# Kernel tuning notes

Hardware: AMD Instinct MI355X
Metric: run time of the kernel (lower is better)

## Reference

```python
import jax, jax.numpy as jnp
import numpy as np

N_LAYERS = 32
D_CONV = 4
D_STATE = 16


def _ln(x, w, b, eps=1e-5):
    mu = jnp.mean(x, axis=-1, keepdims=True)
    var = jnp.mean((x - mu) ** 2, axis=-1, keepdims=True)
    return (x - mu) / jnp.sqrt(var + eps) * w + b


def _mamba(x, in_w, conv_w, conv_b, xproj_w, dt_w, dt_b, A_log, D_skip, out_w):
    # x: (B, L, d_model); standard Mamba mixer (mamba_ssm defaults)
    B, L, _ = x.shape
    d_inner = in_w.shape[0] // 2
    xz = jnp.einsum('bld,ed->ble', x, in_w)  # (B, L, 2*d_inner)
    xs, z = xz[..., :d_inner], xz[..., d_inner:]
    # causal depthwise conv1d (kernel D_CONV) + SiLU
    xp = jnp.pad(xs, ((0, 0), (D_CONV - 1, 0), (0, 0)))
    xc = conv_b + sum(conv_w[:, k] * xp[:, k:k + L, :] for k in range(D_CONV))
    xc = jax.nn.silu(xc)
    dt_rank = dt_w.shape[1]
    dbc = jnp.einsum('bld,nd->bln', xc, xproj_w)  # (B, L, dt_rank + 2*d_state)
    dt = jax.nn.softplus(jnp.einsum('blr,dr->bld', dbc[..., :dt_rank], dt_w) + dt_b)
    Bm = dbc[..., dt_rank:dt_rank + D_STATE]
    Cm = dbc[..., dt_rank + D_STATE:]
    A = -jnp.exp(A_log)  # (d_inner, d_state)

    def step(h, inp):
        dt_t, B_t, C_t, x_t = inp  # (B,d),(B,n),(B,n),(B,d)
        h = jnp.exp(dt_t[..., None] * A) * h + dt_t[..., None] * B_t[:, None, :] * x_t[..., None]
        return h, jnp.einsum('bdn,bn->bd', h, C_t)

    h0 = jnp.zeros((B, d_inner, D_STATE), x.dtype)
    _, ys = jax.lax.scan(step, h0, (jnp.swapaxes(dt, 0, 1), jnp.swapaxes(Bm, 0, 1),
                                    jnp.swapaxes(Cm, 0, 1), jnp.swapaxes(xc, 0, 1)))
    y = jnp.swapaxes(ys, 0, 1) + D_skip * xc
    y = y * jax.nn.silu(z)
    return jnp.einsum('bld,od->blo', y, out_w)


def _forward(hidden_states, proj_w, proj_b, query, ln_w, ln_b, in_w, conv_w, conv_b,
             xproj_w, dt_w, dt_b, A_log, D_skip, out_w, norm_w, norm_b, num_query_token):
    h = jnp.einsum('bli,di->bld', hidden_states, proj_w) + proj_b
    B = h.shape[0]
    h = jnp.concatenate([h, jnp.broadcast_to(query, (B, query.shape[1], query.shape[2]))], axis=1)

    def layer(carry, p):
        hs, res = carry
        lw, lb, iw, cw, cb, xw, dw, db, al, dsk, ow = p
        res = hs + res  # first layer: res starts at 0 == residual=None case
        hs = _mamba(_ln(res, lw, lb), iw, cw, cb, xw, dw, db, al, dsk, ow)
        return (hs, res), None

    (hs, res), _ = jax.lax.scan(layer, (h, jnp.zeros_like(h)),
                                (ln_w, ln_b, in_w, conv_w, conv_b, xproj_w, dt_w, dt_b, A_log, D_skip, out_w))
    out = _ln(hs + res, norm_w, norm_b)
    return out[:, -num_query_token:]


def setup_inputs():
    key = jax.random.key(0)
    B, L, input_dim, d_model, nq = 2, 256, 1408, 512, 7
    d_inner, dt_rank = 2 * d_model, 32  # ceil(d_model/16)
    ks = jax.random.split(key, 9)
    s = 0.02
    return {
        'hidden_states': jax.random.normal(ks[0], (B, L, input_dim), jnp.float32),
        'proj_w': jax.random.normal(ks[1], (d_model, input_dim), jnp.float32) * s,
        'proj_b': jnp.zeros((d_model,), jnp.float32),
        'query': jax.random.uniform(ks[2], (1, nq, d_model), jnp.float32),
        'ln_w': jnp.ones((N_LAYERS, d_model), jnp.float32),
        'ln_b': jnp.zeros((N_LAYERS, d_model), jnp.float32),
        'in_w': jax.random.normal(ks[3], (N_LAYERS, 2 * d_inner, d_model), jnp.float32) * s,
        'conv_w': jax.random.normal(ks[4], (N_LAYERS, d_inner, D_CONV), jnp.float32) * 0.1,
        'conv_b': jnp.zeros((N_LAYERS, d_inner), jnp.float32),
        'xproj_w': jax.random.normal(ks[5], (N_LAYERS, dt_rank + 2 * D_STATE, d_inner), jnp.float32) * s,
        'dt_w': jax.random.normal(ks[6], (N_LAYERS, d_inner, dt_rank), jnp.float32) * s,
        'dt_b': jax.random.normal(ks[7], (N_LAYERS, d_inner), jnp.float32) * 0.1 - 4.0,
        'A_log': jnp.log(jnp.broadcast_to(jnp.arange(1, D_STATE + 1, dtype=jnp.float32), (N_LAYERS, d_inner, D_STATE))),
        'D_skip': jnp.ones((N_LAYERS, d_inner), jnp.float32),
        'out_w': jax.random.normal(ks[8], (N_LAYERS, d_model, d_inner), jnp.float32) * s,
        'norm_w': jnp.ones((d_model,), jnp.float32),
        'norm_b': jnp.zeros((d_model,), jnp.float32),
        'num_query_token': nq,
    }


def reference(hidden_states, proj_w, proj_b, query, ln_w, ln_b, in_w, conv_w, conv_b,
              xproj_w, dt_w, dt_b, A_log, D_skip, out_w, norm_w, norm_b, num_query_token):
    return _forward(hidden_states, proj_w, proj_b, query, ln_w, ln_b, in_w, conv_w, conv_b,
                    xproj_w, dt_w, dt_b, A_log, D_skip, out_w, norm_w, norm_b, num_query_token)
```

## Files before the change

### kernel.cpp

```cpp
#include <hip/hip_runtime.h>

#define DM 512
#define DI 1024
#define LSEQ 263
#define NTOK 526
#define NLAYER 32
#define DTR 32
#define DSTATE 16

typedef __attribute__((ext_vector_type(8))) short bf16x8;
typedef __attribute__((ext_vector_type(4))) short bf16x4;
typedef __attribute__((ext_vector_type(4))) float f32x4;

__device__ __forceinline__ short f2bf(float f) {
  unsigned u = __float_as_uint(f);
  unsigned r = u + 0x7FFFu + ((u >> 16) & 1u);
  return (short)(r >> 16);
}
__device__ __forceinline__ float silu_f(float v) { return v / (1.f + __expf(-v)); }
__device__ __forceinline__ float softplus_f(float x) {
  return fmaxf(x, 0.f) + log1pf(__expf(-fabsf(x)));
}

template<int BM, int BN, int AM, int AN, int MODE>
__global__ __launch_bounds__(256) void gemm_k(
    const float* __restrict__ A, const float* __restrict__ Bw,
    float* __restrict__ C, const float* __restrict__ x0,
    const float* __restrict__ x1, int M, int N, int K)
{
  constexpr int WC = BN / (AN * 16);
  constexpr int TPRA = 256 / BM, EPA = 32 / TPRA;
  constexpr int TPRB = 256 / BN, EPB = 32 / TPRB;
  __shared__ short As[BM][40];
  __shared__ short Bs[BN][40];
  __shared__ float mu_s[BM], rs_s[BM];
  const int tid = threadIdx.x;
  const int lane = tid & 63;
  const int w = tid >> 6;
  const int wm = (w / WC) * (AM * 16), wn = (w % WC) * (AN * 16);
  const int m0 = blockIdx.y * BM, n0 = blockIdx.x * BN;
  const int arow = tid / TPRA, acol = (tid % TPRA) * EPA;
  const int brow = tid / TPRB, bcol = (tid % TPRB) * EPB;
  const int agr = m0 + arow;
  const size_t abase = (size_t)agr * K + acol;
  const size_t bbase = (size_t)(n0 + brow) * K + bcol;

  if constexpr (MODE == 1) {
    for (int r = w; r < BM; r += 4) {
      int row = m0 + r;
      float s = 0.f, ss = 0.f;
      if (row < M) {
        const float4* p = reinterpret_cast<const float4*>(A + (size_t)row * 512 + lane * 8);
        float4 v0 = p[0], v1 = p[1];
        s = v0.x + v0.y + v0.z + v0.w + v1.x + v1.y + v1.z + v1.w;
        ss = v0.x*v0.x + v0.y*v0.y + v0.z*v0.z + v0.w*v0.w
           + v1.x*v1.x + v1.y*v1.y + v1.z*v1.z + v1.w*v1.w;
      }
#pragma unroll
      for (int o = 1; o < 64; o <<= 1) { s += __shfl_xor(s, o); ss += __shfl_xor(ss, o); }
      if (lane == 0) {
        float mean = s * (1.f / 512.f);
        float var = ss * (1.f / 512.f) - mean * mean;
        mu_s[r] = mean;
        rs_s[r] = rsqrtf(var + 1e-5f);
      }
    }
    __syncthreads();
  }

  f32x4 acc[AM][AN] = {};
  float4 pa[2], pb[2], pw[2], pl[2];

  auto loadA = [&](int k0) {
    if (agr < M) {
      const float4* p = reinterpret_cast<const float4*>(A + abase + k0);
      pa[0] = p[0];
      if constexpr (EPA == 8) pa[1] = p[1];
    } else {
      pa[0] = make_float4(0.f, 0.f, 0.f, 0.f);
      pa[1] = make_float4(0.f, 0.f, 0.f, 0.f);
    }
    if constexpr (MODE == 1) {
      const float4* pwp = reinterpret_cast<const float4*>(x0 + k0 + acol);
      const float4* plp = reinterpret_cast<const float4*>(x1 + k0 + acol);
      pw[0] = pwp[0]; pw[1] = pwp[1];
      pl[0] = plp[0]; pl[1] = plp[1];
    }
  };
  auto loadB = [&](int k0) {
    const float4* p = reinterpret_cast<const float4*>(Bw + bbase + k0);
    pb[0] = p[0];
    if constexpr (EPB == 8) pb[1] = p[1];
  };
  auto stage = [&]() {
    float va[8];
    va[0]=pa[0].x; va[1]=pa[0].y; va[2]=pa[0].z; va[3]=pa[0].w;
    if constexpr (EPA == 8) { va[4]=pa[1].x; va[5]=pa[1].y; va[6]=pa[1].z; va[7]=pa[1].w; }
    if constexpr (MODE == 1) {
      float mu = mu_s[arow], rs = rs_s[arow];
      float wv[8] = {pw[0].x,pw[0].y,pw[0].z,pw[0].w,pw[1].x,pw[1].y,pw[1].z,pw[1].w};
      float bv[8] = {pl[0].x,pl[0].y,pl[0].z,pl[0].w,pl[1].x,pl[1].y,pl[1].z,pl[1].w};
#pragma unroll
      for (int j = 0; j < EPA; ++j) va[j] = (va[j] - mu) * rs * wv[j] + bv[j];
    }
    if constexpr (EPA == 8) {
      bf16x8 o;
#pragma unroll
      for (int j = 0; j < 8; ++j) o[j] = f2bf(va[j]);
      *reinterpret_cast<bf16x8*>(&As[arow][acol]) = o;
    } else {
      bf16x4 o;
#pragma unroll
      for (int j = 0; j < 4; ++j) o[j] = f2bf(va[j]);
      *reinterpret_cast<bf16x4*>(&As[arow][acol]) = o;
    }
    float vb[8];
    vb[0]=pb[0].x; vb[1]=pb[0].y; vb[2]=pb[0].z; vb[3]=pb[0].w;
    if constexpr (EPB == 8) { vb[4]=pb[1].x; vb[5]=pb[1].y; vb[6]=pb[1].z; vb[7]=pb[1].w; }
    if constexpr (EPB == 8) {
      bf16x8 o;
#pragma unroll
      for (int j = 0; j < 8; ++j) o[j] = f2bf(vb[j]);
      *reinterpret_cast<bf16x8*>(&Bs[brow][bcol]) = o;
    } else {
      bf16x4 o;
#pragma unroll
      for (int j = 0; j < 4; ++j) o[j] = f2bf(vb[j]);
      *reinterpret_cast<bf16x4*>(&Bs[brow][bcol]) = o;
    }
  };

  loadA(0); loadB(0);
  const int nk = K / 32;
  for (int kk = 0; kk < nk; ++kk) {
    stage();
    __syncthreads();
    if (kk + 1 < nk) { loadA((kk + 1) * 32); loadB((kk + 1) * 32); }
    bf16x8 af[AM], bfr[AN];
#pragma unroll
    for (int i = 0; i < AM; ++i)
      af[i] = *reinterpret_cast<const bf16x8*>(&As[wm + i * 16 + (lane & 15)][(lane >> 4) * 8]);
#pragma unroll
    for (int j = 0; j < AN; ++j)
      bfr[j] = *reinterpret_cast<const bf16x8*>(&Bs[wn + j * 16 + (lane & 15)][(lane >> 4) * 8]);
#pragma unroll
    for (int i = 0; i < AM; ++i)
#pragma unroll
      for (int j = 0; j < AN; ++j)
        acc[i][j] = __builtin_amdgcn_mfma_f32_16x16x32_bf16(af[i], bfr[j], acc[i][j], 0, 0, 0);
    __syncthreads();
  }

#pragma unroll
  for (int i = 0; i < AM; ++i)
#pragma unroll
    for (int j = 0; j < AN; ++j)
#pragma unroll
      for (int r = 0; r < 4; ++r) {
        int row = m0 + wm + i * 16 + ((lane >> 4) << 2) + r;
        int col = n0 + wn + j * 16 + (lane & 15);
        if (row < M) {
          float v = acc[i][j][r];
          if constexpr (MODE == 0) {
            v += x0[col];
            int orow = ((row >> 8) * LSEQ) + (row & 255);
            C[(size_t)orow * N + col] = v;
          } else if constexpr (MODE == 1) {
            C[(size_t)row * N + col] = v;
          } else {
            C[(size_t)row * N + col] += v;
          }
        }
      }
}

__global__ void set_query_kernel(const float* __restrict__ q, float* __restrict__ res) {
  int i = blockIdx.x * 256 + threadIdx.x;
  if (i >= 2 * 7 * DM) return;
  int b = i / (7 * DM);
  int rrem = i - b * 7 * DM;
  int t = rrem / DM, d = rrem - t * DM;
  res[((size_t)b * LSEQ + 256 + t) * DM + d] = q[t * DM + d];
}

__global__ __launch_bounds__(256) void prep_kernel(
    const float* __restrict__ xz,
    const float* __restrict__ conv_w, const float* __restrict__ conv_b,
    const float* __restrict__ xproj_w,
    const float* __restrict__ dt_w, const float* __restrict__ dt_b,
    const float* __restrict__ Dsk,
    float* __restrict__ dt, float* __restrict__ dtx,
    float* __restrict__ w1o, float* __restrict__ w0o,
    float* __restrict__ Bm, float* __restrict__ Cm)
{
  __shared__ float xcs[DI];
  __shared__ float dbc_s[64];
  __shared__ float sp_s[DI];
  const int blk = blockIdx.x;
  const int t = blk % LSEQ;
  const int tid = threadIdx.x;
  const int lane = tid & 63;
  const int w = tid >> 6;
  const int c0 = tid * 4;

  {
    const float4* cwp = reinterpret_cast<const float4*>(conv_w + (size_t)c0 * 4);
    float4 cw0 = cwp[0], cw1 = cwp[1], cw2 = cwp[2], cw3 = cwp[3];
    float4 cb4 = *reinterpret_cast<const float4*>(conv_b + c0);
    float4 D4  = *reinterpret_cast<const float4*>(Dsk + c0);
    float4 xr[4];
#pragma unroll
    for (int k = 0; k < 4; ++k) {
      if (t - 3 + k >= 0)
        xr[k] = *reinterpret_cast<const float4*>(xz + (size_t)(blk - 3 + k) * 2048 + c0);
      else
        xr[k] = make_float4(0.f, 0.f, 0.f, 0.f);
    }
    float xc0 = silu_f(cb4.x + cw0.x*xr[0].x + cw0.y*xr[1].x + cw0.z*xr[2].x + cw0.w*xr[3].x);
    float xc1 = silu_f(cb4.y + cw1.x*xr[0].y + cw1.y*xr[1].y + cw1.z*xr[2].y + cw1.w*xr[3].y);
    float xc2 = silu_f(cb4.z + cw2.x*xr[0].z + cw2.y*xr[1].z + cw2.z*xr[2].z + cw2.w*xr[3].z);
    float xc3 = silu_f(cb4.w + cw3.x*xr[0].w + cw3.y*xr[1].w + cw3.z*xr[2].w + cw3.w*xr[3].w);
    xcs[c0] = xc0; xcs[c0+1] = xc1; xcs[c0+2] = xc2; xcs[c0+3] = xc3;
    float4 zv = *reinterpret_cast<const float4*>(xz + (size_t)blk * 2048 + DI + c0);
    float g0 = silu_f(zv.x), g1 = silu_f(zv.y), g2 = silu_f(zv.z), g3 = silu_f(zv.w);
    *reinterpret_cast<float4*>(w1o + (size_t)blk * DI + c0) = make_float4(g0, g1, g2, g3);
    *reinterpret_cast<float4*>(w0o + (size_t)blk * DI + c0) =
        make_float4(D4.x*xc0*g0, D4.y*xc1*g1, D4.z*xc2*g2, D4.w*xc3*g3);
  }
  __syncthreads();
  {
#pragma unroll 2
    for (int nn = 0; nn < 16; ++nn) {
      int nidx = w * 16 + nn;
      const float4* wr = reinterpret_cast<const float4*>(xproj_w + (size_t)nidx * DI);
      float s = 0.f;
#pragma unroll
      for (int j = 0; j < 4; ++j) {
        float4 wv = wr[j * 64 + lane];
        float4 xv = *reinterpret_cast<const float4*>(&xcs[j * 256 + lane * 4]);
        s += wv.x*xv.x + wv.y*xv.y + wv.z*xv.z + wv.w*xv.w;
      }
#pragma unroll
      for (int o = 1; o < 64; o <<= 1) s += __shfl_xor(s, o);
      if (lane == 0) dbc_s[nidx] = s;
    }
  }
  __syncthreads();
  if (tid < 32) {
    float v = dbc_s[32 + tid];
    if (tid < 16) Bm[(size_t)blk * DSTATE + tid] = v;
    else          Cm[(size_t)blk * DSTATE + (tid - 16)] = v;
  }
  {
    const int rp = tid & 7;
    float4 dv = *reinterpret_cast<const float4*>(&dbc_s[rp * 4]);
#pragma unroll 4
    for (int it = 0; it < 32; ++it) {
      int c = it * 32 + (tid >> 3);
      float4 wv = *reinterpret_cast<const float4*>(dt_w + (size_t)c * DTR + rp * 4);
      float s = wv.x*dv.x + wv.y*dv.y + wv.z*dv.z + wv.w*dv.w;
      s += __shfl_xor(s, 1); s += __shfl_xor(s, 2); s += __shfl_xor(s, 4);
      if (rp == 0) sp_s[c] = s;
    }
  }
  __syncthreads();
  {
    float4 db4 = *reinterpret_cast<const float4*>(dt_b + c0);
    float sp0 = softplus_f(sp_s[c0+0] + db4.x);
    float sp1 = softplus_f(sp_s[c0+1] + db4.y);
    float sp2 = softplus_f(sp_s[c0+2] + db4.z);
    float sp3 = softplus_f(sp_s[c0+3] + db4.w);
    *reinterpret_cast<float4*>(dt  + (size_t)blk * DI + c0) = make_float4(sp0, sp1, sp2, sp3);
    *reinterpret_cast<float4*>(dtx + (size_t)blk * DI + c0) =
        make_float4(sp0*xcs[c0], sp1*xcs[c0+1], sp2*xcs[c0+2], sp3*xcs[c0+3]);
  }
}

__global__ __launch_bounds__(128) void scan_kernel(
    const float* __restrict__ dt, const float* __restrict__ dtx,
    const float* __restrict__ Bm, const float* __restrict__ Cm,
    const float* __restrict__ w1, const float* __restrict__ w0,
    const float* __restrict__ A_log, float* __restrict__ y)
{
  const int blk = blockIdx.x;
  const int b = blk >> 7, cg = blk & 127;
  const int tid = threadIdx.x;
  const int n = tid & 15, cl = tid >> 4;
  const int c = cg * 8 + cl;
  const float Av = -__expf(A_log[(size_t)c * DSTATE + n]);
  float h = 0.f;
  __shared__ float sdt[64][8], sdx[64][8], sw1[64][8], sw0[64][8], sy[64][8];
  __shared__ float sB[64][16], sC[64][16];
  const size_t rb = (size_t)b * LSEQ;
  for (int t0 = 0; t0 < LSEQ; t0 += 64) {
    const int tc = (LSEQ - t0 < 64) ? (LSEQ - t0) : 64;
    __syncthreads();
    for (int i = tid; i < tc * 8; i += 128) {
      int tl = i >> 3, cc = i & 7;
      size_t g = (rb + t0 + tl) * DI + cg * 8 + cc;
      sdt[tl][cc] = dt[g]; sdx[tl][cc] = dtx[g];
      sw1[tl][cc] = w1[g]; sw0[tl][cc] = w0[g];
    }
    for (int i = tid; i < tc * 16; i += 128) {
      int tl = i >> 4, cc = i & 15;
      size_t gb = (rb + t0 + tl) * DSTATE + cc;
      sB[tl][cc] = Bm[gb]; sC[tl][cc] = Cm[gb];
    }
    __syncthreads();
    int tl = 0;
    for (; tl + 4 <= tc; tl += 4) {
      float e0 = __expf(sdt[tl+0][cl] * Av);
      float e1 = __expf(sdt[tl+1][cl] * Av);
      float e2 = __expf(sdt[tl+2][cl] * Av);
      float e3 = __expf(sdt[tl+3][cl] * Av);
      float x0_ = sdx[tl+0][cl] * sB[tl+0][n];
      float x1_ = sdx[tl+1][cl] * sB[tl+1][n];
      float x2_ = sdx[tl+2][cl] * sB[tl+2][n];
      float x3_ = sdx[tl+3][cl] * sB[tl+3][n];
      h = fmaf(e0, h, x0_); float p0 = h * sC[tl+0][n];
      h = fmaf(e1, h, x1_); float p1 = h * sC[tl+1][n];
      h = fmaf(e2, h, x2_); float p2 = h * sC[tl+2][n];
      h = fmaf(e3, h, x3_); float p3 = h * sC[tl+3][n];
      p0 += __shfl_xor(p0, 1); p1 += __shfl_xor(p1, 1); p2 += __shfl_xor(p2, 1); p3 += __shfl_xor(p3, 1);
      p0 += __shfl_xor(p0, 2); p1 += __shfl_xor(p1, 2); p2 += __shfl_xor(p2, 2); p3 += __shfl_xor(p3, 2);
      p0 += __shfl_xor(p0, 4); p1 += __shfl_xor(p1, 4); p2 += __shfl_xor(p2, 4); p3 += __shfl_xor(p3, 4);
      p0 += __shfl_xor(p0, 8); p1 += __shfl_xor(p1, 8); p2 += __shfl_xor(p2, 8); p3 += __shfl_xor(p3, 8);
      if (n == 0) {
        sy[tl+0][cl] = fmaf(p0, sw1[tl+0][cl], sw0[tl+0][cl]);
        sy[tl+1][cl] = fmaf(p1, sw1[tl+1][cl], sw0[tl+1][cl]);
        sy[tl+2][cl] = fmaf(p2, sw1[tl+2][cl], sw0[tl+2][cl]);
        sy[tl+3][cl] = fmaf(p3, sw1[tl+3][cl], sw0[tl+3][cl]);
      }
    }
    for (; tl < tc; ++tl) {
      float e = __expf(sdt[tl][cl] * Av);
      float bx = sdx[tl][cl] * sB[tl][n];
      h = fmaf(e, h, bx);
      float p = h * sC[tl][n];
      p += __shfl_xor(p, 1); p += __shfl_xor(p, 2);
      p += __shfl_xor(p, 4); p += __shfl_xor(p, 8);
      if (n == 0) sy[tl][cl] = fmaf(p, sw1[tl][cl], sw0[tl][cl]);
    }
    __syncthreads();
    for (int i = tid; i < tc * 8; i += 128) {
      int tl2 = i >> 3, cc = i & 7;
      y[(rb + t0 + tl2) * DI + cg * 8 + cc] = sy[tl2][cc];
    }
  }
}

__global__ __launch_bounds__(256) void final_ln_kernel(
    const float* __restrict__ res, const float* __restrict__ w,
    const float* __restrict__ b_, float* __restrict__ out)
{
  const int blk = blockIdx.x;
  const int bb = blk / 7, q = blk % 7;
  const int tid = threadIdx.x;
  const size_t base = ((size_t)bb * LSEQ + 256 + q) * DM;
  float r0 = res[base + tid];
  float r1 = res[base + tid + 256];
  float s = r0 + r1, ss = r0 * r0 + r1 * r1;
#pragma unroll
  for (int o = 1; o < 64; o <<= 1) { s += __shfl_xor(s, o); ss += __shfl_xor(ss, o); }
  __shared__ float sb[4], ssb[4];
  if ((tid & 63) == 0) { sb[tid >> 6] = s; ssb[tid >> 6] = ss; }
  __syncthreads();
  s = sb[0] + sb[1] + sb[2] + sb[3];
  ss = ssb[0] + ssb[1] + ssb[2] + ssb[3];
  float mean = s * (1.f / DM);
  float var = ss * (1.f / DM) - mean * mean;
  float rstd = rsqrtf(var + 1e-5f);
  out[((size_t)bb * 7 + q) * DM + tid] = (r0 - mean) * rstd * w[tid] + b_[tid];
  out[((size_t)bb * 7 + q) * DM + tid + 256] = (r1 - mean) * rstd * w[tid + 256] + b_[tid + 256];
}

extern "C" void kernel_launch(void* const* d_in, const int* in_sizes, int n_in,
                              void* d_out, int out_size, void* d_ws, size_t ws_size,
                              hipStream_t stream)
{
  (void)in_sizes; (void)n_in; (void)out_size; (void)ws_size;
  const float* hidden  = (const float*)d_in[0];
  const float* proj_w  = (const float*)d_in[1];
  const float* proj_b  = (const float*)d_in[2];
  const float* query   = (const float*)d_in[3];
  const float* ln_w    = (const float*)d_in[4];
  const float* ln_b    = (const float*)d_in[5];
  const float* in_w    = (const float*)d_in[6];
  const float* conv_w  = (const float*)d_in[7];
  const float* conv_b  = (const float*)d_in[8];
  const float* xproj_w = (const float*)d_in[9];
  const float* dt_w    = (const float*)d_in[10];
  const float* dt_b    = (const float*)d_in[11];
  const float* A_log   = (const float*)d_in[12];
  const float* D_skip  = (const float*)d_in[13];
  const float* out_w   = (const float*)d_in[14];
  const float* norm_w  = (const float*)d_in[15];
  const float* norm_b  = (const float*)d_in[16];
  float* out = (float*)d_out;

  float* p = (float*)d_ws;
  float* res  = p; p += (size_t)NTOK * DM;
  float* xzb  = p; p += (size_t)NTOK * 2048;
  float* dtb_ = p; p += (size_t)NTOK * DI;
  float* dtxb = p; p += (size_t)NTOK * DI;
  float* w1b  = p; p += (size_t)NTOK * DI;
  float* w0b  = p; p += (size_t)NTOK * DI;
  float* yb   = p; p += (size_t)NTOK * DI;
  float* Bmb  = p; p += (size_t)NTOK * DSTATE;
  float* Cmb  = p; p += (size_t)NTOK * DSTATE;

  gemm_k<64,64,2,2,0><<<dim3(DM / 64, 512 / 64), 256, 0, stream>>>(
      hidden, proj_w, res, proj_b, nullptr, 512, DM, 1408);
  set_query_kernel<<<28, 256, 0, stream>>>(query, res);

  for (int l = 0; l < NLAYER; ++l) {
    gemm_k<64,64,2,2,1><<<dim3(2048 / 64, (NTOK + 63) / 64), 256, 0, stream>>>(
        res, in_w + (size_t)l * 2048 * DM, xzb,
        ln_w + (size_t)l * DM, ln_b + (size_t)l * DM, NTOK, 2048, DM);
    prep_kernel<<<NTOK, 256, 0, stream>>>(
        xzb, conv_w + (size_t)l * DI * 4, conv_b + (size_t)l * DI,
        xproj_w + (size_t)l * 64 * DI, dt_w + (size_t)l * DI * DTR,
        dt_b + (size_t)l * DI, D_skip + (size_t)l * DI,
        dtb_, dtxb, w1b, w0b, Bmb, Cmb);
    scan_kernel<<<256, 128, 0, stream>>>(dtb_, dtxb, Bmb, Cmb, w1b, w0b,
                                         A_log + (size_t)l * DI * DSTATE, yb);
    gemm_k<32,32,1,1,2><<<dim3(DM / 32, (NTOK + 31) / 32), 256, 0, stream>>>(
        yb, out_w + (size_t)l * DM * DI, res, nullptr, nullptr, NTOK, DM, DI);
  }
  final_ln_kernel<<<14, 256, 0, stream>>>(res, norm_w, norm_b, out);
}
```

Baseline: 4.361 ms.

## Pre-pack GEMM operands to bf16 fragment layout and stream via global_load_lds

Weights, hidden states and LayerNorm-ed activations are converted once per call into bf16 tiles laid out in MFMA fragment order. A new GEMM kernel then copies those tiles straight into LDS with global_load_lds, triple-buffered, with no register-side conversion. The scan kernel now writes its output directly in this packed bf16 form, and the output projection uses split-K across four slices with atomicAdd into the residual. This is meant to cut the in-loop fp32-to-bf16 conversion and global load latency, at the cost of extra pack kernels, extra workspace, and non-deterministic atomic accumulation.

```diff
diff --git a/kernel.cpp b/kernel.cpp
--- a/kernel.cpp
+++ b/kernel.cpp
@@ -9,7 +9,6 @@
 #define DSTATE 16
 
 typedef __attribute__((ext_vector_type(8))) short bf16x8;
-typedef __attribute__((ext_vector_type(4))) short bf16x4;
 typedef __attribute__((ext_vector_type(4))) float f32x4;
 
 __device__ __forceinline__ short f2bf(float f) {
@@ -22,153 +21,162 @@
   return fmaxf(x, 0.f) + log1pf(__expf(-fabsf(x)));
 }
 
-template<int BM, int BN, int AM, int AN, int MODE>
-__global__ __launch_bounds__(256) void gemm_k(
-    const float* __restrict__ A, const float* __restrict__ Bw,
-    float* __restrict__ C, const float* __restrict__ x0,
-    const float* __restrict__ x1, int M, int N, int K)
-{
-  constexpr int WC = BN / (AN * 16);
-  constexpr int TPRA = 256 / BM, EPA = 32 / TPRA;
-  constexpr int TPRB = 256 / BN, EPB = 32 / TPRB;
-  __shared__ short As[BM][40];
-  __shared__ short Bs[BN][40];
-  __shared__ float mu_s[BM], rs_s[BM];
+__device__ __forceinline__ void gll16(const void* g, void* l) {
+  __builtin_amdgcn_global_load_lds(
+      (const __attribute__((address_space(1))) unsigned int*)g,
+      (__attribute__((address_space(3))) unsigned int*)l, 16, 0, 0);
+}
+#define WAITV(n) asm volatile("s_waitcnt vmcnt(" #n ")" ::: "memory")
+#define BAR() __builtin_amdgcn_s_barrier()
+
+
+__global__ __launch_bounds__(256) void pack_w(
+    const float* __restrict__ W, short* __restrict__ P,
+    int Nrows, int K, int ntn, int nkc)
+{
+  const int per = ntn * nkc;
+  const int layer = blockIdx.x / per, rem = blockIdx.x % per;
+  const int tn = rem / nkc, kc = rem % nkc;
+  const float* Wl = W + (size_t)layer * Nrows * K;
+  short* Pl = P + (size_t)layer * (size_t)per * 4096;
   const int tid = threadIdx.x;
-  const int lane = tid & 63;
-  const int w = tid >> 6;
-  const int wm = (w / WC) * (AM * 16), wn = (w % WC) * (AN * 16);
-  const int m0 = blockIdx.y * BM, n0 = blockIdx.x * BN;
-  const int arow = tid / TPRA, acol = (tid % TPRA) * EPA;
-  const int brow = tid / TPRB, bcol = (tid % TPRB) * EPB;
-  const int agr = m0 + arow;
-  const size_t abase = (size_t)agr * K + acol;
-  const size_t bbase = (size_t)(n0 + brow) * K + bcol;
-
-  if constexpr (MODE == 1) {
-    for (int r = w; r < BM; r += 4) {
-      int row = m0 + r;
-      float s = 0.f, ss = 0.f;
-      if (row < M) {
-        const float4* p = reinterpret_cast<const float4*>(A + (size_t)row * 512 + lane * 8);
-        float4 v0 = p[0], v1 = p[1];
-        s = v0.x + v0.y + v0.z + v0.w + v1.x + v1.y + v1.z + v1.w;
-        ss = v0.x*v0.x + v0.y*v0.y + v0.z*v0.z + v0.w*v0.w
-           + v1.x*v1.x + v1.y*v1.y + v1.z*v1.z + v1.w*v1.w;
+#pragma unroll
+  for (int h = 0; h < 2; ++h) {
+    int u = h * 256 + tid;
+    int ks = u >> 8, g = (u >> 6) & 3, l = u & 63;
+    int n = tn * 64 + g * 16 + (l & 15);
+    int k = kc * 64 + ks * 32 + (l >> 4) * 8;
+    const float4* src = reinterpret_cast<const float4*>(Wl + (size_t)n * K + k);
+    float4 v0 = src[0], v1 = src[1];
+    bf16x8 o;
+    o[0]=f2bf(v0.x); o[1]=f2bf(v0.y); o[2]=f2bf(v0.z); o[3]=f2bf(v0.w);
+    o[4]=f2bf(v1.x); o[5]=f2bf(v1.y); o[6]=f2bf(v1.z); o[7]=f2bf(v1.w);
+    *reinterpret_cast<bf16x8*>(&Pl[((size_t)(tn * nkc + kc) * 512 + u) * 8]) = o;
+  }
+}
+
+__global__ __launch_bounds__(256) void pack_x(
+    const float* __restrict__ res, const float* __restrict__ lnw,
+    const float* __restrict__ lnb, short* __restrict__ P)
+{
+  __shared__ float mu_s[64], rs_s[64];
+  const int tm = blockIdx.x, tid = threadIdx.x;
+  const int lane = tid & 63, w = tid >> 6;
+  for (int rr = 0; rr < 16; ++rr) {
+    int rl = w * 16 + rr, row = tm * 64 + rl;
+    float s = 0.f, ss = 0.f;
+    if (row < NTOK) {
+      const float4* p = reinterpret_cast<const float4*>(res + (size_t)row * DM + lane * 8);
+      float4 a = p[0], b = p[1];
+      s = a.x+a.y+a.z+a.w+b.x+b.y+b.z+b.w;
+      ss = a.x*a.x+a.y*a.y+a.z*a.z+a.w*a.w + b.x*b.x+b.y*b.y+b.z*b.z+b.w*b.w;
+    }
+#pragma unroll
+    for (int o = 1; o < 64; o <<= 1) { s += __shfl_xor(s, o); ss += __shfl_xor(ss, o); }
+    if (lane == 0) {
+      float mean = s * (1.f / DM);
+      float var = ss * (1.f / DM) - mean * mean;
+      mu_s[rl] = mean; rs_s[rl] = rsqrtf(var + 1e-5f);
+    }
+  }
+  __syncthreads();
+  for (int kc = 0; kc < 8; ++kc) {
+#pragma unroll
+    for (int h = 0; h < 2; ++h) {
+      int u = h * 256 + tid;
+      int ks = u >> 8, g = (u >> 6) & 3, l = u & 63;
+      int rl = g * 16 + (l & 15), row = tm * 64 + rl;
+      int k = kc * 64 + ks * 32 + (l >> 4) * 8;
+      float4 v0 = make_float4(0,0,0,0), v1 = v0;
+      if (row < NTOK) {
+        const float4* p = reinterpret_cast<const float4*>(res + (size_t)row * DM + k);
+        v0 = p[0]; v1 = p[1];
       }
-#pragma unroll
-      for (int o = 1; o < 64; o <<= 1) { s += __shfl_xor(s, o); ss += __shfl_xor(ss, o); }
-      if (lane == 0) {
-        float mean = s * (1.f / 512.f);
-        float var = ss * (1.f / 512.f) - mean * mean;
-        mu_s[r] = mean;
-        rs_s[r] = rsqrtf(var + 1e-5f);
-      }
-    }
-    __syncthreads();
-  }
-
-  f32x4 acc[AM][AN] = {};
-  float4 pa[2], pb[2], pw[2], pl[2];
-
-  auto loadA = [&](int k0) {
-    if (agr < M) {
-      const float4* p = reinterpret_cast<const float4*>(A + abase + k0);
-      pa[0] = p[0];
-      if constexpr (EPA == 8) pa[1] = p[1];
-    } else {
-      pa[0] = make_float4(0.f, 0.f, 0.f, 0.f);
-      pa[1] = make_float4(0.f, 0.f, 0.f, 0.f);
-    }
-    if constexpr (MODE == 1) {
-      const float4* pwp = reinterpret_cast<const float4*>(x0 + k0 + acol);
-      const float4* plp = reinterpret_cast<const float4*>(x1 + k0 + acol);
-      pw[0] = pwp[0]; pw[1] = pwp[1];
-      pl[0] = plp[0]; pl[1] = plp[1];
-    }
+      float mu = mu_s[rl], rs = rs_s[rl];
+      const float4* pw = reinterpret_cast<const float4*>(lnw + k);
+      const float4* pb = reinterpret_cast<const float4*>(lnb + k);
+      float4 w0 = pw[0], w1 = pw[1], b0 = pb[0], b1 = pb[1];
+      bf16x8 o;
+      o[0]=f2bf((v0.x-mu)*rs*w0.x+b0.x); o[1]=f2bf((v0.y-mu)*rs*w0.y+b0.y);
+      o[2]=f2bf((v0.z-mu)*rs*w0.z+b0.z); o[3]=f2bf((v0.w-mu)*rs*w0.w+b0.w);
+      o[4]=f2bf((v1.x-mu)*rs*w1.x+b1.x); o[5]=f2bf((v1.y-mu)*rs*w1.y+b1.y);
+      o[6]=f2bf((v1.z-mu)*rs*w1.z+b1.z); o[7]=f2bf((v1.w-mu)*rs*w1.w+b1.w);
+      *reinterpret_cast<bf16x8*>(&P[((size_t)(tm * 8 + kc) * 512 + u) * 8]) = o;
+    }
+  }
+}
+
+template<int NC, int MODE>
+__global__ __launch_bounds__(256) void gemm_pk(
+    const short* __restrict__ Apk, const short* __restrict__ Bpk,
+    float* __restrict__ C, const float* __restrict__ bias,
+    int M, int N, int nkc)
+{
+  __shared__ short As[3][4096];
+  __shared__ short Bs[3][4096];
+  const int tid = threadIdx.x;
+  const int lane = tid & 63, w = tid >> 6;
+  const int wr = w >> 1, wc = w & 1;
+  const int tn = blockIdx.x, tm = blockIdx.y;
+  const int ck0 = blockIdx.z * NC;
+  const size_t abase = ((size_t)tm * nkc + ck0) * 512 + tid;
+  const size_t bbase = ((size_t)tn * nkc + ck0) * 512 + tid;
+
+  f32x4 acc[2][2] = {};
+
+  auto stage = [&](int t, int s) {
+    const short* ga = Apk + (abase + (size_t)t * 512) * 8;
+    const short* gb = Bpk + (bbase + (size_t)t * 512) * 8;
+    gll16(ga,            &As[s][tid * 8]);
+    gll16(ga + 256 * 8,  &As[s][(256 + tid) * 8]);
+    gll16(gb,            &Bs[s][tid * 8]);
+    gll16(gb + 256 * 8,  &Bs[s][(256 + tid) * 8]);
   };
-  auto loadB = [&](int k0) {
-    const float4* p = reinterpret_cast<const float4*>(Bw + bbase + k0);
-    pb[0] = p[0];
-    if constexpr (EPB == 8) pb[1] = p[1];
+  auto compute = [&](int s) {
+#pragma unroll
+    for (int ks = 0; ks < 2; ++ks) {
+      bf16x8 a0 = *reinterpret_cast<const bf16x8*>(&As[s][(ks*256 + (wr*2+0)*64 + lane) * 8]);
+      bf16x8 a1 = *reinterpret_cast<const bf16x8*>(&As[s][(ks*256 + (wr*2+1)*64 + lane) * 8]);
+      bf16x8 b0 = *reinterpret_cast<const bf16x8*>(&Bs[s][(ks*256 + (wc*2+0)*64 + lane) * 8]);
+      bf16x8 b1 = *reinterpret_cast<const bf16x8*>(&Bs[s][(ks*256 + (wc*2+1)*64 + lane) * 8]);
+      acc[0][0] = __builtin_amdgcn_mfma_f32_16x16x32_bf16(a0, b0, acc[0][0], 0, 0, 0);
+      acc[0][1] = __builtin_amdgcn_mfma_f32_16x16x32_bf16(a0, b1, acc[0][1], 0, 0, 0);
+      acc[1][0] = __builtin_amdgcn_mfma_f32_16x16x32_bf16(a1, b0, acc[1][0], 0, 0, 0);
+      acc[1][1] = __builtin_amdgcn_mfma_f32_16x16x32_bf16(a1, b1, acc[1][1], 0, 0, 0);
+    }
   };
-  auto stage = [&]() {
-    float va[8];
-    va[0]=pa[0].x; va[1]=pa[0].y; va[2]=pa[0].z; va[3]=pa[0].w;
-    if constexpr (EPA == 8) { va[4]=pa[1].x; va[5]=pa[1].y; va[6]=pa[1].z; va[7]=pa[1].w; }
-    if constexpr (MODE == 1) {
-      float mu = mu_s[arow], rs = rs_s[arow];
-      float wv[8] = {pw[0].x,pw[0].y,pw[0].z,pw[0].w,pw[1].x,pw[1].y,pw[1].z,pw[1].w};
-      float bv[8] = {pl[0].x,pl[0].y,pl[0].z,pl[0].w,pl[1].x,pl[1].y,pl[1].z,pl[1].w};
-#pragma unroll
-      for (int j = 0; j < EPA; ++j) va[j] = (va[j] - mu) * rs * wv[j] + bv[j];
-    }
-    if constexpr (EPA == 8) {
-      bf16x8 o;
-#pragma unroll
-      for (int j = 0; j < 8; ++j) o[j] = f2bf(va[j]);
-      *reinterpret_cast<bf16x8*>(&As[arow][acol]) = o;
-    } else {
-      bf16x4 o;
-#pragma unroll
-      for (int j = 0; j < 4; ++j) o[j] = f2bf(va[j]);
-      *reinterpret_cast<bf16x4*>(&As[arow][acol]) = o;
-    }
-    float vb[8];
-    vb[0]=pb[0].x; vb[1]=pb[0].y; vb[2]=pb[0].z; vb[3]=pb[0].w;
-    if constexpr (EPB == 8) { vb[4]=pb[1].x; vb[5]=pb[1].y; vb[6]=pb[1].z; vb[7]=pb[1].w; }
-    if constexpr (EPB == 8) {
-      bf16x8 o;
-#pragma unroll
-      for (int j = 0; j < 8; ++j) o[j] = f2bf(vb[j]);
-      *reinterpret_cast<bf16x8*>(&Bs[brow][bcol]) = o;
-    } else {
-      bf16x4 o;
-#pragma unroll
-      for (int j = 0; j < 4; ++j) o[j] = f2bf(vb[j]);
-      *reinterpret_cast<bf16x4*>(&Bs[brow][bcol]) = o;
-    }
-  };
-
-  loadA(0); loadB(0);
-  const int nk = K / 32;
-  for (int kk = 0; kk < nk; ++kk) {
-    stage();
-    __syncthreads();
-    if (kk + 1 < nk) { loadA((kk + 1) * 32); loadB((kk + 1) * 32); }
-    bf16x8 af[AM], bfr[AN];
-#pragma unroll
-    for (int i = 0; i < AM; ++i)
-      af[i] = *reinterpret_cast<const bf16x8*>(&As[wm + i * 16 + (lane & 15)][(lane >> 4) * 8]);
-#pragma unroll
-    for (int j = 0; j < AN; ++j)
-      bfr[j] = *reinterpret_cast<const bf16x8*>(&Bs[wn + j * 16 + (lane & 15)][(lane >> 4) * 8]);
-#pragma unroll
-    for (int i = 0; i < AM; ++i)
-#pragma unroll
-      for (int j = 0; j < AN; ++j)
-        acc[i][j] = __builtin_amdgcn_mfma_f32_16x16x32_bf16(af[i], bfr[j], acc[i][j], 0, 0, 0);
-    __syncthreads();
-  }
-
-#pragma unroll
-  for (int i = 0; i < AM; ++i)
-#pragma unroll
-    for (int j = 0; j < AN; ++j)
+
+  stage(0, 0); stage(1, 1); stage(2, 2);
+#pragma unroll 1
+  for (int t = 0; t + 3 < NC; ++t) {
+    WAITV(8);
+    BAR();
+    compute(t % 3);
+    BAR();
+    stage(t + 3, t % 3);
+  }
+  WAITV(8); BAR(); compute((NC - 3) % 3);
+  WAITV(4); BAR(); compute((NC - 2) % 3);
+  WAITV(0); BAR(); compute((NC - 1) % 3);
+
+#pragma unroll
+  for (int i = 0; i < 2; ++i)
+#pragma unroll
+    for (int j = 0; j < 2; ++j)
 #pragma unroll
       for (int r = 0; r < 4; ++r) {
-        int row = m0 + wm + i * 16 + ((lane >> 4) << 2) + r;
-        int col = n0 + wn + j * 16 + (lane & 15);
+        int row = tm * 64 + wr * 32 + i * 16 + ((lane >> 4) << 2) + r;
+        int col = tn * 64 + wc * 32 + j * 16 + (lane & 15);
         if (row < M) {
           float v = acc[i][j][r];
           if constexpr (MODE == 0) {
-            v += x0[col];
+            v += bias[col];
             int orow = ((row >> 8) * LSEQ) + (row & 255);
             C[(size_t)orow * N + col] = v;
           } else if constexpr (MODE == 1) {
             C[(size_t)row * N + col] = v;
           } else {
-            C[(size_t)row * N + col] += v;
+            atomicAdd(&C[(size_t)row * N + col], v);
           }
         }
       }
@@ -280,7 +288,7 @@
     const float* __restrict__ dt, const float* __restrict__ dtx,
     const float* __restrict__ Bm, const float* __restrict__ Cm,
     const float* __restrict__ w1, const float* __restrict__ w0,
-    const float* __restrict__ A_log, float* __restrict__ y)
+    const float* __restrict__ A_log, short* __restrict__ ypk)
 {
   const int blk = blockIdx.x;
   const int b = blk >> 7, cg = blk & 127;
@@ -292,6 +300,7 @@
   __shared__ float sdt[64][8], sdx[64][8], sw1[64][8], sw0[64][8], sy[64][8];
   __shared__ float sB[64][16], sC[64][16];
   const size_t rb = (size_t)b * LSEQ;
+  const int kc = cg >> 3, ks = (cg >> 2) & 1, cgrp = cg & 3;
   for (int t0 = 0; t0 < LSEQ; t0 += 64) {
     const int tc = (LSEQ - t0 < 64) ? (LSEQ - t0) : 64;
     __syncthreads();
@@ -342,9 +351,14 @@
       if (n == 0) sy[tl][cl] = fmaf(p, sw1[tl][cl], sw0[tl][cl]);
     }
     __syncthreads();
-    for (int i = tid; i < tc * 8; i += 128) {
-      int tl2 = i >> 3, cc = i & 7;
-      y[(rb + t0 + tl2) * DI + cg * 8 + cc] = sy[tl2][cc];
+    for (int i2 = tid; i2 < tc; i2 += 128) {
+      int r = (int)rb + t0 + i2;
+      int tmr = r >> 6, g = (r >> 4) & 3, rl = r & 15;
+      bf16x8 o;
+#pragma unroll
+      for (int cc = 0; cc < 8; ++cc) o[cc] = f2bf(sy[i2][cc]);
+      size_t unit = ((size_t)(tmr * 16 + kc) * 512) + ks * 256 + g * 64 + cgrp * 16 + rl;
+      *reinterpret_cast<bf16x8*>(&ypk[unit * 8]) = o;
     }
   }
 }
@@ -405,27 +419,38 @@
   float* dtxb = p; p += (size_t)NTOK * DI;
   float* w1b  = p; p += (size_t)NTOK * DI;
   float* w0b  = p; p += (size_t)NTOK * DI;
-  float* yb   = p; p += (size_t)NTOK * DI;
   float* Bmb  = p; p += (size_t)NTOK * DSTATE;
   float* Cmb  = p; p += (size_t)NTOK * DSTATE;
-
-  gemm_k<64,64,2,2,0><<<dim3(DM / 64, 512 / 64), 256, 0, stream>>>(
-      hidden, proj_w, res, proj_b, nullptr, 512, DM, 1408);
+  short* sp = (short*)p;
+  short* inw_pk  = sp; sp += (size_t)NLAYER * 32 * 8 * 4096;
+  short* outw_pk = sp; sp += (size_t)NLAYER * 8 * 16 * 4096;
+  short* projw_pk= sp; sp += (size_t)8 * 22 * 4096;
+  short* hid_pk  = sp; sp += (size_t)8 * 22 * 4096;
+  short* x_pk    = sp; sp += (size_t)9 * 8 * 4096;
+  short* y_pk    = sp; sp += (size_t)9 * 16 * 4096;
+
+  pack_w<<<NLAYER * 32 * 8, 256, 0, stream>>>(in_w,  inw_pk,  2048, 512,  32, 8);
+  pack_w<<<NLAYER * 8 * 16, 256, 0, stream>>>(out_w, outw_pk, 512,  1024, 8, 16);
+  pack_w<<<8 * 22, 256, 0, stream>>>(proj_w, projw_pk, 512, 1408, 8, 22);
+  pack_w<<<8 * 22, 256, 0, stream>>>(hidden, hid_pk,   512, 1408, 8, 22);
+
+  gemm_pk<22, 0><<<dim3(8, 8, 1), 256, 0, stream>>>(
+      hid_pk, projw_pk, res, proj_b, 512, DM, 22);
   set_query_kernel<<<28, 256, 0, stream>>>(query, res);
 
   for (int l = 0; l < NLAYER; ++l) {
-    gemm_k<64,64,2,2,1><<<dim3(2048 / 64, (NTOK + 63) / 64), 256, 0, stream>>>(
-        res, in_w + (size_t)l * 2048 * DM, xzb,
-        ln_w + (size_t)l * DM, ln_b + (size_t)l * DM, NTOK, 2048, DM);
+    pack_x<<<9, 256, 0, stream>>>(res, ln_w + (size_t)l * DM, ln_b + (size_t)l * DM, x_pk);
+    gemm_pk<8, 1><<<dim3(32, 9, 1), 256, 0, stream>>>(
+        x_pk, inw_pk + (size_t)l * 32 * 8 * 4096, xzb, nullptr, NTOK, 2048, 8);
     prep_kernel<<<NTOK, 256, 0, stream>>>(
         xzb, conv_w + (size_t)l * DI * 4, conv_b + (size_t)l * DI,
         xproj_w + (size_t)l * 64 * DI, dt_w + (size_t)l * DI * DTR,
         dt_b + (size_t)l * DI, D_skip + (size_t)l * DI,
         dtb_, dtxb, w1b, w0b, Bmb, Cmb);
     scan_kernel<<<256, 128, 0, stream>>>(dtb_, dtxb, Bmb, Cmb, w1b, w0b,
-                                         A_log + (size_t)l * DI * DSTATE, yb);
-    gemm_k<32,32,1,1,2><<<dim3(DM / 32, (NTOK + 31) / 32), 256, 0, stream>>>(
-        yb, out_w + (size_t)l * DM * DI, res, nullptr, nullptr, NTOK, DM, DI);
+                                         A_log + (size_t)l * DI * DSTATE, y_pk);
+    gemm_pk<4, 2><<<dim3(8, 9, 4), 256, 0, stream>>>(
+        y_pk, outw_pk + (size_t)l * 8 * 16 * 4096, res, nullptr, NTOK, DM, 16);
   }
   final_ln_kernel<<<14, 256, 0, stream>>>(res, norm_w, norm_b, out);
 }
```

New measurement: 3.764 ms. -13.7%, faster.
